# Optimization experiments

Hardware: AMD Instinct MI355X
Metric: run time of the kernel (lower is better)

The kernel has to match this reference:

```python
import jax, jax.numpy as jnp
import numpy as np

TAU = 2.0
BN_EPS = 1e-5
HEADS = 8

# spikingjelly-style Heaviside spike with sigmoid surrogate gradient (alpha=4)
@jax.custom_vjp
def spike(x):
    return (x >= 0.0).astype(x.dtype)

def _spike_fwd(x):
    return (x >= 0.0).astype(x.dtype), x

def _spike_bwd(x, g):
    s = jax.nn.sigmoid(4.0 * x)
    return (g * 4.0 * s * (1.0 - s),)

spike.defvjp(_spike_fwd, _spike_bwd)

def lif(x, thresh):
    """Multi-step LIF (tau=2, decay_input=True, hard reset to 0, detach_reset).
    x: (T, ...) input current; returns spikes of the same shape."""
    def step(v, xt):
        v = v + (xt - v) / TAU          # charge
        s = spike(v - thresh)           # fire
        v = v * (1.0 - jax.lax.stop_gradient(s))  # hard reset, detached
        return v, s
    _, s = jax.lax.scan(step, jnp.zeros_like(x[0]), x)
    return s

def bn(x, gamma, beta, mean, var):
    # inference-mode BatchNorm2d over channel axis 2 of (T,B,C,H,W)
    sh = (1, 1, -1, 1, 1)
    scale = gamma / jnp.sqrt(var + BN_EPS)
    return (x - mean.reshape(sh)) * scale.reshape(sh) + beta.reshape(sh)

def setup_inputs() -> dict:
    key = jax.random.key(0)
    T, B, C, H, W = 4, 16, 512, 16, 16
    ks = jax.random.split(key, 24)
    def wmat(k):
        return jax.random.normal(k, (C, C), jnp.float32) * (1.0 / np.sqrt(C))
    def bnp(k):
        k1, k2, k3, k4 = jax.random.split(k, 4)
        return (jax.random.normal(k1, (C,), jnp.float32) * 0.1 + 1.0,
                jax.random.normal(k2, (C,), jnp.float32) * 0.1,
                jax.random.normal(k3, (C,), jnp.float32) * 0.1,
                jax.random.uniform(k4, (C,), jnp.float32) + 0.5)
    qg, qb, qm, qvar = bnp(ks[1]); kg, kb, km, kvar = bnp(ks[3])
    vg, vb, vm, vvar = bnp(ks[5]); pg, pb, pm, pvar = bnp(ks[8])
    return {
        'x': jax.random.normal(ks[0], (T, B, C, H, W), jnp.float32),
        'wq': wmat(ks[10]), 'qg': qg, 'qb': qb, 'qm': qm, 'qvar': qvar,
        'wk': wmat(ks[11]), 'kg': kg, 'kb': kb, 'km': km, 'kvar': kvar,
        'wv': wmat(ks[12]), 'vg': vg, 'vb': vb, 'vm': vm, 'vvar': vvar,
        'wp': wmat(ks[13]), 'bp': jax.random.normal(ks[14], (C,), jnp.float32) * 0.02,
        'pg': pg, 'pb': pb, 'pm': pm, 'pvar': pvar,
    }

def reference(x, wq, qg, qb, qm, qvar, wk, kg, kb, km, kvar,
              wv, vg, vb, vm, vvar, wp, bp, pg, pb, pm, pvar):
    T, B, C, H, W = x.shape
    dh = C // HEADS
    N = H * W
    identity = x
    xs = lif(x, 1.0)  # shortcut_lif

    def branch(w, g, b, m, v):
        y = jnp.einsum('tbchw,oc->tbohw', xs, w)  # 1x1 conv, no bias
        return lif(bn(y, g, b, m, v), 1.0)

    # (T,B,C,H,W) spikes -> (T,B,heads,N,dh)
    def to_heads(s):
        return s.reshape(T, B, HEADS, dh, N).transpose(0, 1, 2, 4, 3)

    q = to_heads(branch(wq, qg, qb, qm, qvar))
    k = to_heads(branch(wk, kg, kb, km, kvar))
    v = to_heads(branch(wv, vg, vb, vm, vvar))

    kv = (k * v).sum(axis=3, keepdims=True)   # sum over tokens N -> (T,B,h,1,dh)
    kv = lif(kv, 0.5)                          # talking_heads_lif (v_threshold=0.5)

    out = q * kv                               # (T,B,h,N,dh)
    out = out.transpose(0, 1, 2, 4, 3).reshape(T, B, C, H, W)
    out = jnp.einsum('tbchw,oc->tbohw', out, wp) + bp.reshape(1, 1, -1, 1, 1)
    out = bn(out, pg, pb, pm, pvar) + identity
    return out, v
```

## Files before the change

### kernel.cpp

```cpp
#include <hip/hip_runtime.h>
#include <hip/hip_bf16.h>

typedef unsigned short u16;
typedef unsigned int u32;
typedef __attribute__((ext_vector_type(8))) short bh8;
typedef __attribute__((ext_vector_type(4))) short sh4;
typedef __attribute__((ext_vector_type(4))) float f4;

#define T_   4
#define B_   16
#define C_   512
#define N_   256
#define M2_  4096
#define OC3_ 1536

__device__ __forceinline__ u16 f2bf(float f) {
  u32 u = __float_as_uint(f);
  u32 r = (u + 0x7FFFu + ((u >> 16) & 1u)) >> 16;
  return (u16)r;
}
__device__ __forceinline__ void gl_lds16(const void* g, void* l) {
  __builtin_amdgcn_global_load_lds(
      (const __attribute__((address_space(1))) unsigned int*)g,
      (__attribute__((address_space(3))) unsigned int*)l, 16, 0, 0);
}

__global__ void k_prep_w(const float* __restrict__ wq, const float* __restrict__ wk,
                         const float* __restrict__ wv, const float* __restrict__ wp,
                         u16* __restrict__ wcat, u16* __restrict__ wpcat) {
  int id = blockIdx.x * 256 + threadIdx.x;
  int mat = id >> 18;
  int rc  = id & 262143;
  int o = rc >> 9, c = rc & 511;
  const float* src = (mat == 0) ? wq : (mat == 1) ? wk : (mat == 2) ? wv : wp;
  float w = src[rc];
  u16 hu = f2bf(w);
  float hf = __uint_as_float(((u32)hu) << 16);
  u16 lu = f2bf(w - hf);
  if (mat < 3) {
    size_t base = ((size_t)(mat * 512 + o)) * 1024 + c;
    wcat[base] = hu; wcat[base + 512] = lu;
  } else {
    size_t base = (size_t)o * 1024 + c;
    wpcat[base] = hu; wpcat[base + 512] = lu;
  }
}

__global__ void k_prep_c(const float* qg, const float* qb, const float* qm, const float* qv,
                         const float* kg, const float* kb, const float* km, const float* kv2,
                         const float* vg, const float* vb, const float* vm, const float* vv,
                         const float* pg, const float* pb, const float* pm, const float* pv,
                         const float* bp, float* bns, float* pss) {
  int id = blockIdx.x * 256 + threadIdx.x;
  if (id < 1536) {
    int br = id >> 9, c = id & 511;
    const float *g, *b, *m, *va;
    if (br == 0)      { g = qg; b = qb; m = qm; va = qv; }
    else if (br == 1) { g = kg; b = kb; m = km; va = kv2; }
    else              { g = vg; b = vb; m = vm; va = vv; }
    float s = g[c] / sqrtf(va[c] + 1e-5f);
    bns[id * 4 + 0] = s; bns[id * 4 + 1] = m[c]; bns[id * 4 + 2] = b[c];
    bns[id * 4 + 3] = 0.f;
  } else if (id < 2048) {
    int c = id - 1536;
    float s = pg[c] / sqrtf(pv[c] + 1e-5f);
    pss[c * 4 + 0] = bp[c]; pss[c * 4 + 1] = pm[c];
    pss[c * 4 + 2] = s;     pss[c * 4 + 3] = pb[c];
  }
}

__global__ void k_lif_x(const float* __restrict__ x, u16* __restrict__ xs) {
  __shared__ u16 sp[4][64][68];
  int b = blockIdx.z, c0 = blockIdx.y * 64, n0 = blockIdx.x * 64;
  int tid = threadIdx.x;
  int rq = tid >> 4;
  int n4 = (tid & 15) * 4;
  float v[16];
#pragma unroll
  for (int i = 0; i < 16; i++) v[i] = 0.f;
  for (int t = 0; t < 4; t++) {
    const float* xb = x + (((size_t)t * 16 + b) * 512 + c0) * 256 + n0;
#pragma unroll
    for (int i = 0; i < 4; i++) {
      int row = rq + i * 16;
      f4 xv = *(const f4*)(xb + (size_t)row * 256 + n4);
      sh4 sv;
#pragma unroll
      for (int j = 0; j < 4; j++) {
        float vv = v[i * 4 + j];
        vv = vv + (xv[j] - vv) * 0.5f;
        u16 s = 0;
        if (vv >= 1.0f) { s = 0x3F80; vv = 0.f; }
        v[i * 4 + j] = vv;
        sv[j] = (short)s;
      }
      *(sh4*)&sp[t][row][n4] = sv;
    }
  }
  __syncthreads();
  int cp = (tid & 31) * 2;
  int nq = tid >> 5;
  for (int t = 0; t < 4; t++) {
    u16* ob = xs + (((size_t)t * 16 + b) * 256 + n0) * 512 + c0;
#pragma unroll
    for (int i = 0; i < 8; i++) {
      int n = nq + i * 8;
      u32 w = (u32)sp[t][cp][n] | ((u32)sp[t][cp + 1][n] << 16);
      *(u32*)(ob + (size_t)n * 512 + cp) = w;
    }
  }
}

__launch_bounds__(256, 2)
__global__ void k_qkv_gemm(const u16* __restrict__ xs, const u16* __restrict__ wcat,
                           const float* __restrict__ bns, u16* __restrict__ spq) {
  __shared__ u16 lA[128 * 64];
  __shared__ u16 lBh[96 * 64];
  __shared__ u16 lBl[96 * 64];
  int tid = threadIdx.x, lane = tid & 63, wid = tid >> 6;
  int wr = wid >> 1, wc = wid & 1, lr = lane & 15, lq = lane >> 4;
  int m0 = blockIdx.x * 128, o0 = blockIdx.y * 96;

  float scl[3], mn[3], bt[3];
#pragma unroll
  for (int ni = 0; ni < 3; ni++) {
    int ch = o0 + wc * 48 + ni * 16 + lr;
    scl[ni] = bns[ch * 4]; mn[ni] = bns[ch * 4 + 1]; bt[ni] = bns[ch * 4 + 2];
  }

  int srow = tid >> 3;
  u32 sgoff = (u32)(((tid & 7) ^ (srow & 7)) << 4);
  u32 ldst = (u32)tid * 16;

  u32 aoff[4], boff[3];
#pragma unroll
  for (int mi = 0; mi < 4; mi++) {
    int r = wr * 64 + mi * 16 + lr;
    aoff[mi] = r * 128 + ((lq ^ (r & 7)) << 4);
  }
#pragma unroll
  for (int ni = 0; ni < 3; ni++) {
    int r = wc * 48 + ni * 16 + lr;
    boff[ni] = r * 128 + ((lq ^ (r & 7)) << 4);
  }

  float vst[4][3][4];
#pragma unroll
  for (int a = 0; a < 4; a++)
#pragma unroll
    for (int b = 0; b < 3; b++)
#pragma unroll
      for (int c = 0; c < 4; c++) vst[a][b][c] = 0.f;

  const char* Bb = (const char*)wcat + (size_t)o0 * 2048;

  for (int t = 0; t < 4; t++) {
    f4 acc[4][3];
#pragma unroll
    for (int a = 0; a < 4; a++)
#pragma unroll
      for (int b = 0; b < 3; b++) { acc[a][b][0] = 0.f; acc[a][b][1] = 0.f; acc[a][b][2] = 0.f; acc[a][b][3] = 0.f; }

    const char* Ab = (const char*)xs + ((size_t)t * M2_ + m0) * 1024;
    for (int ks = 0; ks < 8; ks++) {
      u32 kb = (u32)ks * 128;
#pragma unroll
      for (int r = 0; r < 4; r++)
        gl_lds16(Ab + (size_t)(r * 32 + srow) * 1024 + kb + sgoff, (char*)lA + r * 4096 + ldst);
#pragma unroll
      for (int r = 0; r < 3; r++) {
        gl_lds16(Bb + (size_t)(r * 32 + srow) * 2048 + kb + sgoff, (char*)lBh + r * 4096 + ldst);
        gl_lds16(Bb + (size_t)(r * 32 + srow) * 2048 + 1024 + kb + sgoff, (char*)lBl + r * 4096 + ldst);
      }
      __syncthreads();
#pragma unroll
      for (int h = 0; h < 2; h++) {
        u32 hx = (u32)h << 6;
        bh8 af[4], bf[3], lf[3];
#pragma unroll
        for (int mi = 0; mi < 4; mi++)
          af[mi] = *(const bh8*)((const char*)lA + (aoff[mi] ^ hx));
#pragma unroll
        for (int ni = 0; ni < 3; ni++) {
          bf[ni] = *(const bh8*)((const char*)lBh + (boff[ni] ^ hx));
          lf[ni] = *(const bh8*)((const char*)lBl + (boff[ni] ^ hx));
        }
#pragma unroll
        for (int mi = 0; mi < 4; mi++)
#pragma unroll
          for (int ni = 0; ni < 3; ni++)
            acc[mi][ni] = __builtin_amdgcn_mfma_f32_16x16x32_bf16(af[mi], bf[ni], acc[mi][ni], 0, 0, 0);
#pragma unroll
        for (int mi = 0; mi < 4; mi++)
#pragma unroll
          for (int ni = 0; ni < 3; ni++)
            acc[mi][ni] = __builtin_amdgcn_mfma_f32_16x16x32_bf16(af[mi], lf[ni], acc[mi][ni], 0, 0, 0);
      }
      __syncthreads();
    }
#pragma unroll
    for (int mi = 0; mi < 4; mi++)
#pragma unroll
      for (int ni = 0; ni < 3; ni++)
#pragma unroll
        for (int j = 0; j < 4; j++) {
          float y = acc[mi][ni][j];
          y = (y - mn[ni]) * scl[ni] + bt[ni];
          float vv = vst[mi][ni][j];
          vv = vv + (y - vv) * 0.5f;
          u16 s = 0;
          if (vv >= 1.0f) { s = 0x3F80; vv = 0.f; }
          vst[mi][ni][j] = vv;
          int r = m0 + wr * 64 + mi * 16 + lq * 4 + j;
          int o = o0 + wc * 48 + ni * 16 + lr;
          spq[((size_t)t * M2_ + r) * OC3_ + o] = s;
        }
  }
}

__global__ void k_kvv(const u16* __restrict__ spq, float* __restrict__ vout,
                      int* __restrict__ kvp) {
  int tb = blockIdx.x >> 3, nc = blockIdx.x & 7;
  int tid = threadIdx.x;
  const char* base = (const char*)spq + ((size_t)tb * 256 + nc * 32) * 3072;
  int c = tid * 2, h = c >> 6, d = c & 63;
  float* vo = vout + (((size_t)tb * 8 + h) * 256 + nc * 32) * 64 + d;
  int cnt0 = 0, cnt1 = 0;
  for (int n = 0; n < 32; n++) {
    u32 kk = *(const u32*)(base + (size_t)n * 3072 + 1024 + c * 2);
    u32 vv = *(const u32*)(base + (size_t)n * 3072 + 2048 + c * 2);
    u32 a = kk & vv;
    cnt0 += (a & 0xFFFFu) ? 1 : 0;
    cnt1 += (a >> 16) ? 1 : 0;
    float2 w;
    w.x = (vv & 0xFFFFu) ? 1.f : 0.f;
    w.y = (vv >> 16) ? 1.f : 0.f;
    *(float2*)(vo + (size_t)n * 64) = w;
  }
  kvp[((tb * 8 + nc) << 9) + c]     = cnt0;
  kvp[((tb * 8 + nc) << 9) + c + 1] = cnt1;
}

__global__ void k_tlif(const int* __restrict__ kvp, unsigned char* __restrict__ mask) {
  int id = blockIdx.x * 256 + threadIdx.x;
  int b = id >> 9, c = id & 511;
  float v = 0.f;
  for (int t = 0; t < 4; t++) {
    int tb = t * 16 + b;
    int s = 0;
#pragma unroll
    for (int nc = 0; nc < 8; nc++) s += kvp[((tb * 8 + nc) << 9) + c];
    float xx = (float)s;
    v = v + (xx - v) * 0.5f;
    unsigned char sp = 0;
    if (v >= 0.5f) { sp = 1; v = 0.f; }
    mask[tb * 512 + c] = sp;
  }
}

__launch_bounds__(256, 2)
__global__ void k_proj_gemm(const u16* __restrict__ spq, const unsigned char* __restrict__ mask,
                            const u16* __restrict__ wpc, const float* __restrict__ pss,
                            const float* __restrict__ x, float* __restrict__ out) {
  __shared__ u16 lA[128 * 64];
  __shared__ u16 lBh[128 * 64];
  __shared__ u16 lBl[128 * 64];
  __shared__ u16 lm[512];
  int tid = threadIdx.x, lane = tid & 63, wid = tid >> 6;
  int wr = wid >> 1, wc = wid & 1, lr = lane & 15, lq = lane >> 4;
  int m0 = blockIdx.x * 128, o0 = blockIdx.y * 128;
  int tb = m0 >> 8;

  lm[tid]       = mask[tb * 512 + tid]       ? (u16)0xFFFF : (u16)0;
  lm[tid + 256] = mask[tb * 512 + tid + 256] ? (u16)0xFFFF : (u16)0;

  int srow = tid >> 3;
  u32 sgoff = (u32)(((tid & 7) ^ (srow & 7)) << 4);
  u32 ldst = (u32)tid * 16;

  u32 aoff[4], boff[4];
#pragma unroll
  for (int mi = 0; mi < 4; mi++) {
    int r = wr * 64 + mi * 16 + lr;
    aoff[mi] = r * 128 + ((lq ^ (r & 7)) << 4);
  }
#pragma unroll
  for (int ni = 0; ni < 4; ni++) {
    int r = wc * 64 + ni * 16 + lr;
    boff[ni] = r * 128 + ((lq ^ (r & 7)) << 4);
  }

  f4 acc[4][4];
#pragma unroll
  for (int a = 0; a < 4; a++)
#pragma unroll
    for (int b = 0; b < 4; b++) { acc[a][b][0] = 0.f; acc[a][b][1] = 0.f; acc[a][b][2] = 0.f; acc[a][b][3] = 0.f; }

  const char* Ab = (const char*)spq + (size_t)m0 * 3072;
  const char* Bb = (const char*)wpc + (size_t)o0 * 2048;

  for (int ks = 0; ks < 8; ks++) {
    u32 kb = (u32)ks * 128;
#pragma unroll
    for (int r = 0; r < 4; r++) {
      gl_lds16(Ab + (size_t)(r * 32 + srow) * 3072 + kb + sgoff, (char*)lA + r * 4096 + ldst);
      gl_lds16(Bb + (size_t)(r * 32 + srow) * 2048 + kb + sgoff, (char*)lBh + r * 4096 + ldst);
      gl_lds16(Bb + (size_t)(r * 32 + srow) * 2048 + 1024 + kb + sgoff, (char*)lBl + r * 4096 + ldst);
    }
    __syncthreads();
#pragma unroll
    for (int h = 0; h < 2; h++) {
      u32 hx = (u32)h << 6;
      bh8 mq = *(const bh8*)((const char*)lm + kb + (h << 6) + lq * 16);
      bh8 af[4], bf[4], lf[4];
#pragma unroll
      for (int mi = 0; mi < 4; mi++) {
        af[mi] = *(const bh8*)((const char*)lA + (aoff[mi] ^ hx));
        af[mi] = af[mi] & mq;
      }
#pragma unroll
      for (int ni = 0; ni < 4; ni++) {
        bf[ni] = *(const bh8*)((const char*)lBh + (boff[ni] ^ hx));
        lf[ni] = *(const bh8*)((const char*)lBl + (boff[ni] ^ hx));
      }
#pragma unroll
      for (int mi = 0; mi < 4; mi++)
#pragma unroll
        for (int ni = 0; ni < 4; ni++)
          acc[mi][ni] = __builtin_amdgcn_mfma_f32_16x16x32_bf16(af[mi], bf[ni], acc[mi][ni], 0, 0, 0);
#pragma unroll
      for (int mi = 0; mi < 4; mi++)
#pragma unroll
        for (int ni = 0; ni < 4; ni++)
          acc[mi][ni] = __builtin_amdgcn_mfma_f32_16x16x32_bf16(af[mi], lf[ni], acc[mi][ni], 0, 0, 0);
    }
    __syncthreads();
  }
#pragma unroll
  for (int mi = 0; mi < 4; mi++)
#pragma unroll
    for (int ni = 0; ni < 4; ni++) {
      int o = o0 + wc * 64 + ni * 16 + lr;
      f4 ps = *(const f4*)&pss[o * 4];
      int n = (m0 & 255) + wr * 64 + mi * 16 + lq * 4;
      size_t idx = (size_t)tb * 131072 + (size_t)o * 256 + n;
      f4 xv = *(const f4*)&x[idx];
      f4 res;
#pragma unroll
      for (int j = 0; j < 4; j++) {
        float u = acc[mi][ni][j] + ps[0];
        u = (u - ps[1]) * ps[2] + ps[3];
        res[j] = u + xv[j];
      }
      *(f4*)&out[idx] = res;
    }
}

extern "C" void kernel_launch(void* const* d_in, const int* in_sizes, int n_in,
                              void* d_out, int out_size, void* d_ws, size_t ws_size,
                              hipStream_t stream) {
  const float* x  = (const float*)d_in[0];
  const float* wq = (const float*)d_in[1];
  const float* qg = (const float*)d_in[2];
  const float* qb = (const float*)d_in[3];
  const float* qm = (const float*)d_in[4];
  const float* qv = (const float*)d_in[5];
  const float* wk = (const float*)d_in[6];
  const float* kg = (const float*)d_in[7];
  const float* kb = (const float*)d_in[8];
  const float* km = (const float*)d_in[9];
  const float* kv = (const float*)d_in[10];
  const float* wv = (const float*)d_in[11];
  const float* vg = (const float*)d_in[12];
  const float* vb = (const float*)d_in[13];
  const float* vm = (const float*)d_in[14];
  const float* vv = (const float*)d_in[15];
  const float* wp = (const float*)d_in[16];
  const float* bp = (const float*)d_in[17];
  const float* pg = (const float*)d_in[18];
  const float* pb = (const float*)d_in[19];
  const float* pm = (const float*)d_in[20];
  const float* pv = (const float*)d_in[21];

  char* w = (char*)d_ws;
  u16*  XS    = (u16*)(w + 0);
  u16*  SPQ   = (u16*)(w + 16777216);
  u16*  WCAT  = (u16*)(w + 67108864);
  u16*  WPCAT = (u16*)(w + 70254592);
  float* BNS  = (float*)(w + 71303168);
  float* PSS  = (float*)(w + 71327744);
  int*   KVP  = (int*)(w + 71335936);
  unsigned char* MASK = (unsigned char*)(w + 72384512);

  float* out  = (float*)d_out;
  float* vout = out + 8388608;

  k_prep_w<<<4096, 256, 0, stream>>>(wq, wk, wv, wp, WCAT, WPCAT);
  k_prep_c<<<8, 256, 0, stream>>>(qg, qb, qm, qv, kg, kb, km, kv,
                                  vg, vb, vm, vv, pg, pb, pm, pv, bp, BNS, PSS);
  k_lif_x<<<dim3(4, 8, 16), 256, 0, stream>>>(x, XS);
  k_qkv_gemm<<<dim3(32, 16), 256, 0, stream>>>(XS, WCAT, BNS, SPQ);
  k_kvv<<<512, 256, 0, stream>>>(SPQ, vout, KVP);
  k_tlif<<<32, 256, 0, stream>>>(KVP, MASK);
  k_proj_gemm<<<dim3(128, 4), 256, 0, stream>>>(SPQ, MASK, WPCAT, PSS, x, out);
}
```

Baseline: 216.5 us.

## Double-buffer GEMM LDS loads, split spike buffers, fuse v output and prep kernels

Both GEMMs now double-buffer their global-to-LDS staging, using explicit vmcnt waits and barriers so the next K slice loads while MFMAs run on the current one. The QKV GEMM flattens its time and K loops into one pipelined loop and writes q spikes, k/v spikes and the float v output directly, which takes the v write out of k_kvv. The two prep kernels are merged into one launch. The projection GEMM uses 64-wide output tiles, doubling the grid, and reads a compact q buffer. The cost is more LDS per block (80KB for QKV), which may limit occupancy, plus scattered stores for v in the epilogue.

```diff
diff --git a/kernel.cpp b/kernel.cpp
--- a/kernel.cpp
+++ b/kernel.cpp
@@ -12,7 +12,6 @@
 #define C_   512
 #define N_   256
 #define M2_  4096
-#define OC3_ 1536
 
 __device__ __forceinline__ u16 f2bf(float f) {
   u32 u = __float_as_uint(f);
@@ -25,47 +24,49 @@
       (__attribute__((address_space(3))) unsigned int*)l, 16, 0, 0);
 }
 
-__global__ void k_prep_w(const float* __restrict__ wq, const float* __restrict__ wk,
-                         const float* __restrict__ wv, const float* __restrict__ wp,
-                         u16* __restrict__ wcat, u16* __restrict__ wpcat) {
+__global__ void k_prep(const float* __restrict__ wq, const float* __restrict__ wk,
+                       const float* __restrict__ wv, const float* __restrict__ wp,
+                       const float* qg, const float* qb, const float* qm, const float* qv,
+                       const float* kg, const float* kb, const float* km, const float* kv2,
+                       const float* vg, const float* vb, const float* vm, const float* vv,
+                       const float* pg, const float* pb, const float* pm, const float* pv,
+                       const float* bp,
+                       u16* __restrict__ wcat, u16* __restrict__ wpcat,
+                       float* bns, float* pss) {
   int id = blockIdx.x * 256 + threadIdx.x;
-  int mat = id >> 18;
-  int rc  = id & 262143;
-  int o = rc >> 9, c = rc & 511;
-  const float* src = (mat == 0) ? wq : (mat == 1) ? wk : (mat == 2) ? wv : wp;
-  float w = src[rc];
-  u16 hu = f2bf(w);
-  float hf = __uint_as_float(((u32)hu) << 16);
-  u16 lu = f2bf(w - hf);
-  if (mat < 3) {
-    size_t base = ((size_t)(mat * 512 + o)) * 1024 + c;
-    wcat[base] = hu; wcat[base + 512] = lu;
+  if (id < 1048576) {
+    int mat = id >> 18;
+    int rc  = id & 262143;
+    int o = rc >> 9, c = rc & 511;
+    const float* src = (mat == 0) ? wq : (mat == 1) ? wk : (mat == 2) ? wv : wp;
+    float w = src[rc];
+    u16 hu = f2bf(w);
+    float hf = __uint_as_float(((u32)hu) << 16);
+    u16 lu = f2bf(w - hf);
+    if (mat < 3) {
+      size_t base = ((size_t)(mat * 512 + o)) * 1024 + c;
+      wcat[base] = hu; wcat[base + 512] = lu;
+    } else {
+      size_t base = (size_t)o * 1024 + c;
+      wpcat[base] = hu; wpcat[base + 512] = lu;
+    }
   } else {
-    size_t base = (size_t)o * 1024 + c;
-    wpcat[base] = hu; wpcat[base + 512] = lu;
-  }
-}
-
-__global__ void k_prep_c(const float* qg, const float* qb, const float* qm, const float* qv,
-                         const float* kg, const float* kb, const float* km, const float* kv2,
-                         const float* vg, const float* vb, const float* vm, const float* vv,
-                         const float* pg, const float* pb, const float* pm, const float* pv,
-                         const float* bp, float* bns, float* pss) {
-  int id = blockIdx.x * 256 + threadIdx.x;
-  if (id < 1536) {
-    int br = id >> 9, c = id & 511;
-    const float *g, *b, *m, *va;
-    if (br == 0)      { g = qg; b = qb; m = qm; va = qv; }
-    else if (br == 1) { g = kg; b = kb; m = km; va = kv2; }
-    else              { g = vg; b = vb; m = vm; va = vv; }
-    float s = g[c] / sqrtf(va[c] + 1e-5f);
-    bns[id * 4 + 0] = s; bns[id * 4 + 1] = m[c]; bns[id * 4 + 2] = b[c];
-    bns[id * 4 + 3] = 0.f;
-  } else if (id < 2048) {
-    int c = id - 1536;
-    float s = pg[c] / sqrtf(pv[c] + 1e-5f);
-    pss[c * 4 + 0] = bp[c]; pss[c * 4 + 1] = pm[c];
-    pss[c * 4 + 2] = s;     pss[c * 4 + 3] = pb[c];
+    int j = id - 1048576;
+    if (j < 1536) {
+      int br = j >> 9, c = j & 511;
+      const float *g, *b, *m, *va;
+      if (br == 0)      { g = qg; b = qb; m = qm; va = qv; }
+      else if (br == 1) { g = kg; b = kb; m = km; va = kv2; }
+      else              { g = vg; b = vb; m = vm; va = vv; }
+      float s = g[c] / sqrtf(va[c] + 1e-5f);
+      bns[j * 4 + 0] = s; bns[j * 4 + 1] = m[c]; bns[j * 4 + 2] = b[c];
+      bns[j * 4 + 3] = 0.f;
+    } else if (j < 2048) {
+      int c = j - 1536;
+      float s = pg[c] / sqrtf(pv[c] + 1e-5f);
+      pss[c * 4 + 0] = bp[c]; pss[c * 4 + 1] = pm[c];
+      pss[c * 4 + 2] = s;     pss[c * 4 + 3] = pb[c];
+    }
   }
 }
 
@@ -113,10 +114,10 @@
 
 __launch_bounds__(256, 2)
 __global__ void k_qkv_gemm(const u16* __restrict__ xs, const u16* __restrict__ wcat,
-                           const float* __restrict__ bns, u16* __restrict__ spq) {
-  __shared__ u16 lA[128 * 64];
-  __shared__ u16 lBh[96 * 64];
-  __shared__ u16 lBl[96 * 64];
+                           const float* __restrict__ bns,
+                           u16* __restrict__ qs, u16* __restrict__ kvsp,
+                           float* __restrict__ vout) {
+  __shared__ char lds[81920];
   int tid = threadIdx.x, lane = tid & 63, wid = tid >> 6;
   int wr = wid >> 1, wc = wid & 1, lr = lane & 15, lq = lane >> 4;
   int m0 = blockIdx.x * 128, o0 = blockIdx.y * 96;
@@ -144,6 +145,23 @@
     boff[ni] = r * 128 + ((lq ^ (r & 7)) << 4);
   }
 
+  const char* Bb = (const char*)wcat + (size_t)o0 * 2048;
+
+  auto STAGE = [&](int buf, int step) {
+    int t = step >> 3;
+    u32 kb = (u32)(step & 7) * 128;
+    const char* Ab = (const char*)xs + ((size_t)t * M2_ + m0) * 1024;
+    char* L = lds + buf * 40960;
+#pragma unroll
+    for (int r2 = 0; r2 < 4; r2++)
+      gl_lds16(Ab + (size_t)(r2 * 32 + srow) * 1024 + kb + sgoff, L + r2 * 4096 + ldst);
+#pragma unroll
+    for (int r2 = 0; r2 < 3; r2++) {
+      gl_lds16(Bb + (size_t)(r2 * 32 + srow) * 2048 + kb + sgoff, L + 16384 + r2 * 4096 + ldst);
+      gl_lds16(Bb + (size_t)(r2 * 32 + srow) * 2048 + 1024 + kb + sgoff, L + 28672 + r2 * 4096 + ldst);
+    }
+  };
+
   float vst[4][3][4];
 #pragma unroll
   for (int a = 0; a < 4; a++)
@@ -152,90 +170,99 @@
 #pragma unroll
       for (int c = 0; c < 4; c++) vst[a][b][c] = 0.f;
 
-  const char* Bb = (const char*)wcat + (size_t)o0 * 2048;
-
-  for (int t = 0; t < 4; t++) {
-    f4 acc[4][3];
-#pragma unroll
-    for (int a = 0; a < 4; a++)
-#pragma unroll
-      for (int b = 0; b < 3; b++) { acc[a][b][0] = 0.f; acc[a][b][1] = 0.f; acc[a][b][2] = 0.f; acc[a][b][3] = 0.f; }
-
-    const char* Ab = (const char*)xs + ((size_t)t * M2_ + m0) * 1024;
-    for (int ks = 0; ks < 8; ks++) {
-      u32 kb = (u32)ks * 128;
-#pragma unroll
-      for (int r = 0; r < 4; r++)
-        gl_lds16(Ab + (size_t)(r * 32 + srow) * 1024 + kb + sgoff, (char*)lA + r * 4096 + ldst);
-#pragma unroll
-      for (int r = 0; r < 3; r++) {
-        gl_lds16(Bb + (size_t)(r * 32 + srow) * 2048 + kb + sgoff, (char*)lBh + r * 4096 + ldst);
-        gl_lds16(Bb + (size_t)(r * 32 + srow) * 2048 + 1024 + kb + sgoff, (char*)lBl + r * 4096 + ldst);
+  f4 acc[4][3];
+  STAGE(0, 0);
+  int cur = 0;
+  for (int step = 0; step < 32; ++step) {
+    int ks = step & 7;
+    if (ks == 0) {
+#pragma unroll
+      for (int a = 0; a < 4; a++)
+#pragma unroll
+        for (int b = 0; b < 3; b++) { acc[a][b][0] = 0.f; acc[a][b][1] = 0.f; acc[a][b][2] = 0.f; acc[a][b][3] = 0.f; }
+    }
+    if (step < 31) {
+      STAGE(cur ^ 1, step + 1);
+      asm volatile("s_waitcnt vmcnt(10)" ::: "memory");
+    } else {
+      asm volatile("s_waitcnt vmcnt(0)" ::: "memory");
+    }
+    __builtin_amdgcn_s_barrier();
+    __builtin_amdgcn_sched_barrier(0);
+    const char* L = lds + cur * 40960;
+#pragma unroll
+    for (int h = 0; h < 2; h++) {
+      u32 hx = (u32)h << 6;
+      bh8 af[4], bf[3], lf[3];
+#pragma unroll
+      for (int mi = 0; mi < 4; mi++)
+        af[mi] = *(const bh8*)(L + (aoff[mi] ^ hx));
+#pragma unroll
+      for (int ni = 0; ni < 3; ni++) {
+        bf[ni] = *(const bh8*)(L + 16384 + (boff[ni] ^ hx));
+        lf[ni] = *(const bh8*)(L + 28672 + (boff[ni] ^ hx));
       }
-      __syncthreads();
-#pragma unroll
-      for (int h = 0; h < 2; h++) {
-        u32 hx = (u32)h << 6;
-        bh8 af[4], bf[3], lf[3];
-#pragma unroll
-        for (int mi = 0; mi < 4; mi++)
-          af[mi] = *(const bh8*)((const char*)lA + (aoff[mi] ^ hx));
-#pragma unroll
-        for (int ni = 0; ni < 3; ni++) {
-          bf[ni] = *(const bh8*)((const char*)lBh + (boff[ni] ^ hx));
-          lf[ni] = *(const bh8*)((const char*)lBl + (boff[ni] ^ hx));
-        }
-#pragma unroll
-        for (int mi = 0; mi < 4; mi++)
-#pragma unroll
-          for (int ni = 0; ni < 3; ni++)
-            acc[mi][ni] = __builtin_amdgcn_mfma_f32_16x16x32_bf16(af[mi], bf[ni], acc[mi][ni], 0, 0, 0);
-#pragma unroll
-        for (int mi = 0; mi < 4; mi++)
-#pragma unroll
-          for (int ni = 0; ni < 3; ni++)
-            acc[mi][ni] = __builtin_amdgcn_mfma_f32_16x16x32_bf16(af[mi], lf[ni], acc[mi][ni], 0, 0, 0);
-      }
-      __syncthreads();
-    }
-#pragma unroll
-    for (int mi = 0; mi < 4; mi++)
-#pragma unroll
-      for (int ni = 0; ni < 3; ni++)
-#pragma unroll
-        for (int j = 0; j < 4; j++) {
-          float y = acc[mi][ni][j];
-          y = (y - mn[ni]) * scl[ni] + bt[ni];
-          float vv = vst[mi][ni][j];
-          vv = vv + (y - vv) * 0.5f;
-          u16 s = 0;
-          if (vv >= 1.0f) { s = 0x3F80; vv = 0.f; }
-          vst[mi][ni][j] = vv;
-          int r = m0 + wr * 64 + mi * 16 + lq * 4 + j;
-          int o = o0 + wc * 48 + ni * 16 + lr;
-          spq[((size_t)t * M2_ + r) * OC3_ + o] = s;
-        }
-  }
-}
-
-__global__ void k_kvv(const u16* __restrict__ spq, float* __restrict__ vout,
-                      int* __restrict__ kvp) {
+#pragma unroll
+      for (int mi = 0; mi < 4; mi++)
+#pragma unroll
+        for (int ni = 0; ni < 3; ni++)
+          acc[mi][ni] = __builtin_amdgcn_mfma_f32_16x16x32_bf16(af[mi], bf[ni], acc[mi][ni], 0, 0, 0);
+#pragma unroll
+      for (int mi = 0; mi < 4; mi++)
+#pragma unroll
+        for (int ni = 0; ni < 3; ni++)
+          acc[mi][ni] = __builtin_amdgcn_mfma_f32_16x16x32_bf16(af[mi], lf[ni], acc[mi][ni], 0, 0, 0);
+    }
+    if (ks == 7) {
+      int t = step >> 3;
+#pragma unroll
+      for (int mi = 0; mi < 4; mi++)
+#pragma unroll
+        for (int ni = 0; ni < 3; ni++)
+#pragma unroll
+          for (int j = 0; j < 4; j++) {
+            float y = acc[mi][ni][j];
+            y = (y - mn[ni]) * scl[ni] + bt[ni];
+            float vv = vst[mi][ni][j];
+            vv = vv + (y - vv) * 0.5f;
+            u16 s = 0;
+            if (vv >= 1.0f) { s = 0x3F80; vv = 0.f; }
+            vst[mi][ni][j] = vv;
+            int r = wr * 64 + mi * 16 + lq * 4 + j;
+            int rg = m0 + r;
+            int o = o0 + wc * 48 + ni * 16 + lr;
+            size_t rowg = (size_t)t * M2_ + rg;
+            if (o < 512) {
+              qs[rowg * 512 + o] = s;
+            } else {
+              kvsp[rowg * 1024 + (o - 512)] = s;
+              if (o >= 1024) {
+                int cq = o - 1024, hh = cq >> 6, d = cq & 63;
+                int tb = (int)(rowg >> 8);
+                int n = rg & 255;
+                vout[(((size_t)tb * 8 + hh) * 256 + n) * 64 + d] = s ? 1.0f : 0.0f;
+              }
+            }
+          }
+    }
+    __builtin_amdgcn_sched_barrier(0);
+    __builtin_amdgcn_s_barrier();
+    cur ^= 1;
+  }
+}
+
+__global__ void k_kvv(const u16* __restrict__ kvsp, int* __restrict__ kvp) {
   int tb = blockIdx.x >> 3, nc = blockIdx.x & 7;
   int tid = threadIdx.x;
-  const char* base = (const char*)spq + ((size_t)tb * 256 + nc * 32) * 3072;
-  int c = tid * 2, h = c >> 6, d = c & 63;
-  float* vo = vout + (((size_t)tb * 8 + h) * 256 + nc * 32) * 64 + d;
+  const char* base = (const char*)kvsp + ((size_t)tb * 256 + nc * 32) * 2048;
+  int c = tid * 2;
   int cnt0 = 0, cnt1 = 0;
   for (int n = 0; n < 32; n++) {
-    u32 kk = *(const u32*)(base + (size_t)n * 3072 + 1024 + c * 2);
-    u32 vv = *(const u32*)(base + (size_t)n * 3072 + 2048 + c * 2);
+    u32 kk = *(const u32*)(base + (size_t)n * 2048 + c * 2);
+    u32 vv = *(const u32*)(base + (size_t)n * 2048 + 1024 + c * 2);
     u32 a = kk & vv;
     cnt0 += (a & 0xFFFFu) ? 1 : 0;
     cnt1 += (a >> 16) ? 1 : 0;
-    float2 w;
-    w.x = (vv & 0xFFFFu) ? 1.f : 0.f;
-    w.y = (vv >> 16) ? 1.f : 0.f;
-    *(float2*)(vo + (size_t)n * 64) = w;
   }
   kvp[((tb * 8 + nc) << 9) + c]     = cnt0;
   kvp[((tb * 8 + nc) << 9) + c + 1] = cnt1;
@@ -259,16 +286,14 @@
 }
 
 __launch_bounds__(256, 2)
-__global__ void k_proj_gemm(const u16* __restrict__ spq, const unsigned char* __restrict__ mask,
+__global__ void k_proj_gemm(const u16* __restrict__ qs, const unsigned char* __restrict__ mask,
                             const u16* __restrict__ wpc, const float* __restrict__ pss,
                             const float* __restrict__ x, float* __restrict__ out) {
-  __shared__ u16 lA[128 * 64];
-  __shared__ u16 lBh[128 * 64];
-  __shared__ u16 lBl[128 * 64];
-  __shared__ u16 lm[512];
+  __shared__ char lds[66560];
+  u16* lm = (u16*)(lds + 65536);
   int tid = threadIdx.x, lane = tid & 63, wid = tid >> 6;
   int wr = wid >> 1, wc = wid & 1, lr = lane & 15, lq = lane >> 4;
-  int m0 = blockIdx.x * 128, o0 = blockIdx.y * 128;
+  int m0 = blockIdx.x * 128, o0 = blockIdx.y * 64;
   int tb = m0 >> 8;
 
   lm[tid]       = mask[tb * 512 + tid]       ? (u16)0xFFFF : (u16)0;
@@ -278,69 +303,89 @@
   u32 sgoff = (u32)(((tid & 7) ^ (srow & 7)) << 4);
   u32 ldst = (u32)tid * 16;
 
-  u32 aoff[4], boff[4];
+  u32 aoff[4], boff[2];
 #pragma unroll
   for (int mi = 0; mi < 4; mi++) {
     int r = wr * 64 + mi * 16 + lr;
     aoff[mi] = r * 128 + ((lq ^ (r & 7)) << 4);
   }
 #pragma unroll
-  for (int ni = 0; ni < 4; ni++) {
-    int r = wc * 64 + ni * 16 + lr;
+  for (int ni = 0; ni < 2; ni++) {
+    int r = wc * 32 + ni * 16 + lr;
     boff[ni] = r * 128 + ((lq ^ (r & 7)) << 4);
   }
 
-  f4 acc[4][4];
+  const char* Ab = (const char*)qs + (size_t)m0 * 1024;
+  const char* Bb = (const char*)wpc + (size_t)o0 * 2048;
+
+  auto STAGE = [&](int buf, int step) {
+    u32 kb = (u32)step * 128;
+    char* L = lds + buf * 32768;
+#pragma unroll
+    for (int r2 = 0; r2 < 4; r2++)
+      gl_lds16(Ab + (size_t)(r2 * 32 + srow) * 1024 + kb + sgoff, L + r2 * 4096 + ldst);
+#pragma unroll
+    for (int r2 = 0; r2 < 2; r2++) {
+      gl_lds16(Bb + (size_t)(r2 * 32 + srow) * 2048 + kb + sgoff, L + 16384 + r2 * 4096 + ldst);
+      gl_lds16(Bb + (size_t)(r2 * 32 + srow) * 2048 + 1024 + kb + sgoff, L + 24576 + r2 * 4096 + ldst);
+    }
+  };
+
+  f4 acc[4][2];
 #pragma unroll
   for (int a = 0; a < 4; a++)
 #pragma unroll
-    for (int b = 0; b < 4; b++) { acc[a][b][0] = 0.f; acc[a][b][1] = 0.f; acc[a][b][2] = 0.f; acc[a][b][3] = 0.f; }
-
-  const char* Ab = (const char*)spq + (size_t)m0 * 3072;
-  const char* Bb = (const char*)wpc + (size_t)o0 * 2048;
-
-  for (int ks = 0; ks < 8; ks++) {
-    u32 kb = (u32)ks * 128;
-#pragma unroll
-    for (int r = 0; r < 4; r++) {
-      gl_lds16(Ab + (size_t)(r * 32 + srow) * 3072 + kb + sgoff, (char*)lA + r * 4096 + ldst);
-      gl_lds16(Bb + (size_t)(r * 32 + srow) * 2048 + kb + sgoff, (char*)lBh + r * 4096 + ldst);
-      gl_lds16(Bb + (size_t)(r * 32 + srow) * 2048 + 1024 + kb + sgoff, (char*)lBl + r * 4096 + ldst);
-    }
-    __syncthreads();
+    for (int b = 0; b < 2; b++) { acc[a][b][0] = 0.f; acc[a][b][1] = 0.f; acc[a][b][2] = 0.f; acc[a][b][3] = 0.f; }
+
+  __syncthreads();
+  STAGE(0, 0);
+  int cur = 0;
+  for (int step = 0; step < 8; ++step) {
+    u32 kb = (u32)step * 128;
+    if (step < 7) {
+      STAGE(cur ^ 1, step + 1);
+      asm volatile("s_waitcnt vmcnt(8)" ::: "memory");
+    } else {
+      asm volatile("s_waitcnt vmcnt(0)" ::: "memory");
+    }
+    __builtin_amdgcn_s_barrier();
+    __builtin_amdgcn_sched_barrier(0);
+    const char* L = lds + cur * 32768;
 #pragma unroll
     for (int h = 0; h < 2; h++) {
       u32 hx = (u32)h << 6;
       bh8 mq = *(const bh8*)((const char*)lm + kb + (h << 6) + lq * 16);
-      bh8 af[4], bf[4], lf[4];
+      bh8 af[4], bf[2], lf[2];
 #pragma unroll
       for (int mi = 0; mi < 4; mi++) {
-        af[mi] = *(const bh8*)((const char*)lA + (aoff[mi] ^ hx));
+        af[mi] = *(const bh8*)(L + (aoff[mi] ^ hx));
         af[mi] = af[mi] & mq;
       }
 #pragma unroll
-      for (int ni = 0; ni < 4; ni++) {
-        bf[ni] = *(const bh8*)((const char*)lBh + (boff[ni] ^ hx));
-        lf[ni] = *(const bh8*)((const char*)lBl + (boff[ni] ^ hx));
+      for (int ni = 0; ni < 2; ni++) {
+        bf[ni] = *(const bh8*)(L + 16384 + (boff[ni] ^ hx));
+        lf[ni] = *(const bh8*)(L + 24576 + (boff[ni] ^ hx));
       }
 #pragma unroll
       for (int mi = 0; mi < 4; mi++)
 #pragma unroll
-        for (int ni = 0; ni < 4; ni++)
+        for (int ni = 0; ni < 2; ni++)
           acc[mi][ni] = __builtin_amdgcn_mfma_f32_16x16x32_bf16(af[mi], bf[ni], acc[mi][ni], 0, 0, 0);
 #pragma unroll
       for (int mi = 0; mi < 4; mi++)
 #pragma unroll
-        for (int ni = 0; ni < 4; ni++)
+        for (int ni = 0; ni < 2; ni++)
           acc[mi][ni] = __builtin_amdgcn_mfma_f32_16x16x32_bf16(af[mi], lf[ni], acc[mi][ni], 0, 0, 0);
     }
-    __syncthreads();
+    __builtin_amdgcn_sched_barrier(0);
+    __builtin_amdgcn_s_barrier();
+    cur ^= 1;
   }
 #pragma unroll
   for (int mi = 0; mi < 4; mi++)
 #pragma unroll
-    for (int ni = 0; ni < 4; ni++) {
-      int o = o0 + wc * 64 + ni * 16 + lr;
+    for (int ni = 0; ni < 2; ni++) {
+      int o = o0 + wc * 32 + ni * 16 + lr;
       f4 ps = *(const f4*)&pss[o * 4];
       int n = (m0 & 255) + wr * 64 + mi * 16 + lq * 4;
       size_t idx = (size_t)tb * 131072 + (size_t)o * 256 + n;
@@ -384,7 +429,8 @@
 
   char* w = (char*)d_ws;
   u16*  XS    = (u16*)(w + 0);
-  u16*  SPQ   = (u16*)(w + 16777216);
+  u16*  QS    = (u16*)(w + 16777216);
+  u16*  KVSP  = (u16*)(w + 33554432);
   u16*  WCAT  = (u16*)(w + 67108864);
   u16*  WPCAT = (u16*)(w + 70254592);
   float* BNS  = (float*)(w + 71303168);
@@ -395,12 +441,12 @@
   float* out  = (float*)d_out;
   float* vout = out + 8388608;
 
-  k_prep_w<<<4096, 256, 0, stream>>>(wq, wk, wv, wp, WCAT, WPCAT);
-  k_prep_c<<<8, 256, 0, stream>>>(qg, qb, qm, qv, kg, kb, km, kv,
-                                  vg, vb, vm, vv, pg, pb, pm, pv, bp, BNS, PSS);
+  k_prep<<<4104, 256, 0, stream>>>(wq, wk, wv, wp, qg, qb, qm, qv, kg, kb, km, kv,
+                                   vg, vb, vm, vv, pg, pb, pm, pv, bp,
+                                   WCAT, WPCAT, BNS, PSS);
   k_lif_x<<<dim3(4, 8, 16), 256, 0, stream>>>(x, XS);
-  k_qkv_gemm<<<dim3(32, 16), 256, 0, stream>>>(XS, WCAT, BNS, SPQ);
-  k_kvv<<<512, 256, 0, stream>>>(SPQ, vout, KVP);
+  k_qkv_gemm<<<dim3(32, 16), 256, 0, stream>>>(XS, WCAT, BNS, QS, KVSP, vout);
+  k_kvv<<<512, 256, 0, stream>>>(KVSP, KVP);
   k_tlif<<<32, 256, 0, stream>>>(KVP, MASK);
-  k_proj_gemm<<<dim3(128, 4), 256, 0, stream>>>(SPQ, MASK, WPCAT, PSS, x, out);
-}
+  k_proj_gemm<<<dim3(128, 8), 256, 0, stream>>>(QS, MASK, WPCAT, PSS, x, out);
+}
```

After: 248.3 us. 14.7% more time.
